# Optimization experiments

Measured on AMD Instinct MI355X. Metric: run time of the kernel, lower is better.

## Reference

```python
import jax, jax.numpy as jnp
import numpy as np

B, C, H, W = 1, 512, 64, 64
HEADS, DH = 8, 64
DI = HEADS * DH          # 512 = heads * dim_head
SW = 8                   # sliding window size
CB = 16                  # compress block size
SB = 2                   # selection block size
NSEL = 2                 # num selected blocks
N = H * W                # 4096 tokens
NCB = N // CB            # 256 compress blocks
NFB = N // SB            # 2048 fine (selection) blocks
NEG = jnp.finfo(jnp.float32).min


def setup_inputs() -> dict:
    key = jax.random.key(0)
    ks = jax.random.split(key, 24)
    rn = lambda k, shape, s=0.03: jax.random.normal(k, shape, jnp.float32) * s
    return dict(
        x=jax.random.normal(ks[0], (B, C, H, W), jnp.float32),
        w_in=rn(ks[1], (C, C)), b_in=jnp.zeros((C,), jnp.float32),
        g_norm=jnp.ones((C,), jnp.float32),
        wq=rn(ks[2], (DI, C)), wk=rn(ks[3], (DI, C)), wv=rn(ks[4], (DI, C)),
        k_pos=rn(ks[5], (HEADS, CB, DH), 0.02), v_pos=rn(ks[6], (HEADS, CB, DH), 0.02),
        mem_k=rn(ks[7], (HEADS, 1, DH), 0.02), mem_v=rn(ks[8], (HEADS, 1, DH), 0.02),
        kc_w1=rn(ks[9], (CB * DH, CB * DH)), kc_b1=jnp.zeros((CB * DH,), jnp.float32),
        kc_w2=rn(ks[10], (DH, CB * DH)), kc_b2=jnp.zeros((DH,), jnp.float32),
        vc_w1=rn(ks[11], (CB * DH, CB * DH)), vc_b1=jnp.zeros((CB * DH,), jnp.float32),
        vc_w2=rn(ks[12], (DH, CB * DH)), vc_b2=jnp.zeros((DH,), jnp.float32),
        w_strat=rn(ks[13], (3 * HEADS, C)), b_strat=jnp.zeros((3 * HEADS,), jnp.float32),
        w_comb=rn(ks[14], (C, DI)),
        w_out=rn(ks[15], (C, C)), b_out=jnp.zeros((C,), jnp.float32),
    )


def _rope(x):
    # rotary-embedding-torch default: theta=10000, interleaved pairs
    d = x.shape[-1]
    inv = 1.0 / (10000.0 ** (jnp.arange(0, d, 2, dtype=jnp.float32) / d))
    ang = jnp.arange(x.shape[-2], dtype=jnp.float32)[:, None] * inv  # (n, d/2)
    cos = jnp.repeat(jnp.cos(ang), 2, axis=-1)
    sin = jnp.repeat(jnp.sin(ang), 2, axis=-1)
    xp = x.reshape(x.shape[:-1] + (d // 2, 2))
    xr = jnp.stack((-xp[..., 1], xp[..., 0]), axis=-1).reshape(x.shape)
    return x * cos + xr * sin


def reference(x, w_in, b_in, g_norm, wq, wk, wv, k_pos, v_pos, mem_k, mem_v,
              kc_w1, kc_b1, kc_w2, kc_b2, vc_w1, vc_b1, vc_w2, vc_b2,
              w_strat, b_strat, w_comb, w_out, b_out):
    scale = DH ** -0.5
    # proj_in (1x1 conv) then flatten to sequence (b, n, c); residual uses this
    xs = jnp.einsum('bchw,oc->bohw', x, w_in) + b_in[None, :, None, None]
    seq = xs.reshape(B, C, N).transpose(0, 2, 1)
    # RMSNorm
    h = seq * jax.lax.rsqrt(jnp.mean(seq * seq, -1, keepdims=True) + 1e-6) * g_norm
    # qkv -> (b, heads, n, d)
    q = (h @ wq.T).reshape(B, N, HEADS, DH).transpose(0, 2, 1, 3)
    k = (h @ wk.T).reshape(B, N, HEADS, DH).transpose(0, 2, 1, 3)
    v = (h @ wv.T).reshape(B, N, HEADS, DH).transpose(0, 2, 1, 3)

    # ---- 1. compressed attention (block compression MLP + mem kv) ----
    kin = (k + jnp.tile(k_pos, (1, NCB, 1))[None]).reshape(B, HEADS, NCB, CB * DH)
    vin = (v + jnp.tile(v_pos, (1, NCB, 1))[None]).reshape(B, HEADS, NCB, CB * DH)
    ck = jax.nn.relu(kin @ kc_w1.T + kc_b1) @ kc_w2.T + kc_b2   # (b,h,NCB,d)
    cv = jax.nn.relu(vin @ vc_w1.T + vc_b1) @ vc_w2.T + vc_b2
    ck = jnp.concatenate([jnp.broadcast_to(mem_k[None], (B, HEADS, 1, DH)), ck], axis=2)
    cv = jnp.concatenate([jnp.broadcast_to(mem_v[None], (B, HEADS, 1, DH)), cv], axis=2)
    ck_seq = jnp.concatenate([jnp.array([-1]), (jnp.arange(NCB) + 1) * CB - 1])
    cmask = ck_seq[None, :] < jnp.arange(N)[:, None]             # (N, NCB+1), True=attend
    csim = jnp.einsum('bhid,bhjd->bhij', q, ck) * scale
    csim = jnp.where(cmask[None, None], csim, NEG)
    compressed_out = jnp.einsum('bhij,bhjd->bhid', jax.nn.softmax(csim, axis=-1), cv)

    # rotary positions for fine + sliding branches
    rq, rk = _rope(q), _rope(k)

    # ---- 2. fine selection attention ----
    # importance at fine-block granularity; since SB divides CB, each fine block
    # maps to exactly one compress block (equivalent to repeat->mask->mean in torch)
    imp = csim[..., 1:]                                          # drop mem kv logits
    fb_of = jnp.arange(NFB) // (CB // SB)
    imp_fine = imp[..., fb_of]                                   # (b,h,N,NFB)
    blk_causal = jnp.arange(NFB)[None, :] < (jnp.arange(N) // SB)[:, None]
    imp_fine = jnp.where(blk_causal[None, None], imp_fine, -jnp.inf)
    logits = jnp.concatenate([jnp.full((B, HEADS, N, 1), -1e3, jnp.float32), imp_fine], axis=-1)
    probs = jax.nn.softmax(logits, axis=-1)[..., 1:]             # (b,h,N,NFB)
    sel_val, sel_idx = jax.lax.top_k(probs, NSEL)                # (b,h,N,NSEL)
    diag_idx = jnp.broadcast_to((jnp.arange(N) // SB)[None, None, :, None], (B, HEADS, N, 1))
    sel_idx = jnp.concatenate([sel_idx, diag_idx], axis=-1)      # append own (diagonal) block
    fmask_sel = jnp.repeat((sel_val > 1e-10)[..., None], SB, axis=-1)   # (b,h,N,NSEL,SB)
    diag_mask = jnp.arange(SB)[None, :] <= (jnp.arange(N) % SB)[:, None]  # within-block causal
    diag_mask = jnp.broadcast_to(diag_mask[None, None, :, None, :], (B, HEADS, N, 1, SB))
    fmask = jnp.concatenate([fmask_sel, diag_mask], axis=-2).reshape(B, HEADS, N, (NSEL + 1) * SB)
    fk_blk = rk.reshape(B, HEADS, NFB, SB, DH)
    fv_blk = v.reshape(B, HEADS, NFB, SB, DH)
    idx = sel_idx.reshape(B, HEADS, N * (NSEL + 1))[..., None, None]
    fk = jnp.take_along_axis(fk_blk, idx, axis=2).reshape(B, HEADS, N, (NSEL + 1) * SB, DH)
    fv = jnp.take_along_axis(fv_blk, idx, axis=2).reshape(B, HEADS, N, (NSEL + 1) * SB, DH)
    fsim = jnp.einsum('bhid,bhijd->bhij', rq, fk) * scale
    fsim = jnp.where(fmask, fsim, NEG)
    fine_out = jnp.einsum('bhij,bhijd->bhid', jax.nn.softmax(fsim, axis=-1), fv)

    # ---- 3. sliding window attention (causal, exact window: 0 <= i-j <= SW) ----
    kp = jnp.pad(rk, ((0, 0), (0, 0), (SW, 0), (0, 0)))
    vp = jnp.pad(v, ((0, 0), (0, 0), (SW, 0), (0, 0)))
    widx = jnp.arange(N)[:, None] + jnp.arange(SW + 1)[None, :]  # indices into padded seq
    kw = kp[:, :, widx]                                          # (b,h,N,SW+1,d)
    vw = vp[:, :, widx]
    wvalid = (jnp.arange(N)[:, None] - SW + jnp.arange(SW + 1)[None, :]) >= 0
    ssim = jnp.einsum('bhid,bhijd->bhij', rq, kw) * scale
    ssim = jnp.where(wvalid[None, None], ssim, NEG)
    slide_out = jnp.einsum('bhij,bhijd->bhid', jax.nn.softmax(ssim, axis=-1), vw)

    # ---- combine the three strategies with learned sigmoid gates ----
    gates = jax.nn.sigmoid(h @ w_strat.T + b_strat).reshape(B, N, HEADS, 3).transpose(0, 2, 1, 3)
    out = gates[..., 0:1] * compressed_out + gates[..., 1:2] * fine_out + gates[..., 2:3] * slide_out
    out = out.transpose(0, 2, 1, 3).reshape(B, N, DI) @ w_comb.T  # merge heads + combine
    out2d = out.transpose(0, 2, 1).reshape(B, C, H, W)
    return jnp.einsum('bchw,oc->bohw', out2d, w_out) + b_out[None, :, None, None] + xs
```

## Files before the change

### kernel.cpp

```cpp
#include <hip/hip_runtime.h>
#include <hip/hip_bf16.h>
#include <math.h>

typedef __attribute__((ext_vector_type(8))) short s8v;
typedef __attribute__((ext_vector_type(8))) _Float16 h8v;
typedef __attribute__((ext_vector_type(4))) float f4v;
typedef __hip_bfloat16 bf16;

#define NEGF (-3.40282346638528859812e+38f)
#define QSMEM 20480
#define BSMEM 20480

enum { EPI_F32 = 0, EPI_BIAS, EPI_BRELU_BF16, EPI_BF16, EPI_FINAL };

__device__ __forceinline__ float wred_sum(float v) {
#pragma unroll
  for (int m = 1; m < 64; m <<= 1) v += __shfl_xor(v, m, 64);
  return v;
}

template <int EPI>
__device__ __forceinline__ void bgemm_body(char* smem, int bx, int by, int bz,
    const bf16* __restrict__ A, const bf16* __restrict__ B, void* __restrict__ C,
    int K, int ldC, long sA, long sB, long sC,
    const float* __restrict__ bias, const void* __restrict__ aux) {
  short (*Ahs)[2560] = (short(*)[2560])smem;
  short (*Bhs)[2560] = (short(*)[2560])(smem + 2 * 2560 * 2);
  const short* ah = (const short*)A + (long)bz * sA;
  const short* bh = (const short*)B + (long)bz * sB;
  int tid = threadIdx.x;
  int wv_ = tid >> 6, lane = tid & 63;
  int lrow = tid >> 2, lcol = (tid & 3) << 3;
  int lidx = lrow * 40 + lcol;
  long abase = (long)(bx * 64 + lrow) * K + lcol;
  long bbase = (long)(by * 64 + lrow) * K + lcol;
  int frow = lane & 15, fk = (lane >> 4) << 3;
  int aoff = (wv_ * 16 + frow) * 40 + fk;
  f4v acc[4] = {};
  {
    s8v avh = *(const s8v*)&ah[abase];
    s8v bvh = *(const s8v*)&bh[bbase];
    *(s8v*)&Ahs[0][lidx] = avh;
    *(s8v*)&Bhs[0][lidx] = bvh;
  }
  __syncthreads();
  int nit = K >> 5, buf = 0;
  s8v rAa, rAb, rBa, rBb;
  if (nit > 1) {
    rAa = *(const s8v*)&ah[abase + 32];
    rAb = *(const s8v*)&bh[bbase + 32];
  }
#define B_DSMFMA                                                       \
  {                                                                    \
    s8v afh = *(const s8v*)&Ahs[buf][aoff];                            \
    _Pragma("unroll") for (int nt = 0; nt < 4; nt++) {                 \
      s8v bfh = *(const s8v*)&Bhs[buf][(nt * 16 + frow) * 40 + fk];    \
      acc[nt] = __builtin_amdgcn_mfma_f32_16x16x32_bf16(afh, bfh, acc[nt], 0, 0, 0); \
    }                                                                  \
  }
  for (int it = 0; it < nit; it += 2) {
    if (it + 2 < nit) {
      long ko = (long)(it + 2) << 5;
      rBa = *(const s8v*)&ah[abase + ko];
      rBb = *(const s8v*)&bh[bbase + ko];
    }
    B_DSMFMA
    if (it + 1 < nit) {
      *(s8v*)&Ahs[buf ^ 1][lidx] = rAa;
      *(s8v*)&Bhs[buf ^ 1][lidx] = rAb;
      __syncthreads();
      buf ^= 1;
      if (it + 3 < nit) {
        long ko = (long)(it + 3) << 5;
        rAa = *(const s8v*)&ah[abase + ko];
        rAb = *(const s8v*)&bh[bbase + ko];
      }
      B_DSMFMA
      if (it + 2 < nit) {
        *(s8v*)&Ahs[buf ^ 1][lidx] = rBa;
        *(s8v*)&Bhs[buf ^ 1][lidx] = rBb;
        __syncthreads();
        buf ^= 1;
      }
    }
  }
#undef B_DSMFMA
  int rb = bx * 64 + wv_ * 16 + ((lane >> 4) << 2);
#pragma unroll
  for (int nt = 0; nt < 4; nt++) {
    int gn = by * 64 + nt * 16 + (lane & 15);
#pragma unroll
    for (int rg = 0; rg < 4; rg++) {
      int gm = rb + rg;
      float v = acc[nt][rg];
      long ci = (long)bz * sC + (long)gm * ldC + gn;
      if (EPI == EPI_F32) ((float*)C)[ci] = v;
      else if (EPI == EPI_BIAS) ((float*)C)[ci] = v + bias[gn];
      else if (EPI == EPI_BRELU_BF16) ((bf16*)C)[ci] = __float2bfloat16(fmaxf(v + bias[gn], 0.f));
      else if (EPI == EPI_BF16) ((bf16*)C)[ci] = __float2bfloat16(v);
      else if (EPI == EPI_FINAL)
        ((float*)C)[ci] = v + bias[gm] + ((const float*)aux)[(long)gn * 512 + gm];
    }
  }
}


#define HX_DECL                                                     \
  short* L = (short*)smem;                                          \
  const int MS = 64 * 40;                                           \
  int tid = threadIdx.x;                                            \
  int wv = tid >> 6, lane = tid & 63;                               \
  int lrow = tid >> 2, lcol = (tid & 3) << 3;                       \
  int frow = lane & 15, fk = (lane >> 4) << 3;                      \
  int aoff = (wv * 16 + frow) * 40 + fk;                            \
  int soff = lrow * 40 + lcol;                                      \
  f4v acc0[4] = {}, accx[4] = {}, acc2[4] = {};

#define HX_STAGE0                                                   \
  {                                                                 \
    *(h8v*)&L[0 * MS + soff] = *(const h8v*)&Ah[abase];             \
    *(h8v*)&L[1 * MS + soff] = *(const h8v*)&Al[abase];             \
    *(h8v*)&L[2 * MS + soff] = *(const h8v*)&Bh[bbase];             \
    *(h8v*)&L[3 * MS + soff] = *(const h8v*)&Bl[bbase];             \
  }                                                                 \
  __syncthreads();

#define HX_DSMFMA                                                   \
  {                                                                 \
    h8v ah = *(const h8v*)&L[aoff];                                 \
    h8v al = *(const h8v*)&L[MS + aoff];                            \
    _Pragma("unroll") for (int nt = 0; nt < 4; nt++) {              \
      int bo = 2 * MS + (nt * 16 + frow) * 40 + fk;                 \
      h8v bh = *(const h8v*)&L[bo];                                 \
      h8v bl = *(const h8v*)&L[bo + MS];                            \
      acc0[nt] = __builtin_amdgcn_mfma_f32_16x16x32_f16(ah, bh, acc0[nt], 0, 0, 0); \
      accx[nt] = __builtin_amdgcn_mfma_f32_16x16x32_f16(ah, bl, accx[nt], 0, 0, 0); \
      accx[nt] = __builtin_amdgcn_mfma_f32_16x16x32_f16(al, bh, accx[nt], 0, 0, 0); \
      acc2[nt] = __builtin_amdgcn_mfma_f32_16x16x32_f16(al, bl, acc2[nt], 0, 0, 0); \
    }                                                               \
  }

#define HX_LOOP(NIT)                                                \
  h8v rAa, rAb, rAc, rAd, rBa, rBb, rBc, rBd;                       \
  if ((NIT) > 1) {                                                  \
    rAa = *(const h8v*)&Ah[abase + 32];                             \
    rAb = *(const h8v*)&Al[abase + 32];                             \
    rAc = *(const h8v*)&Bh[bbase + 32];                             \
    rAd = *(const h8v*)&Bl[bbase + 32];                             \
  }                                                                 \
  for (int it = 0; it < (NIT); it += 2) {                           \
    if (it + 2 < (NIT)) {                                           \
      long ko = (long)(it + 2) << 5;                                \
      rBa = *(const h8v*)&Ah[abase + ko];                           \
      rBb = *(const h8v*)&Al[abase + ko];                           \
      rBc = *(const h8v*)&Bh[bbase + ko];                           \
      rBd = *(const h8v*)&Bl[bbase + ko];                           \
    }                                                               \
    HX_DSMFMA                                                       \
    if (it + 1 < (NIT)) {                                           \
      __syncthreads();                                              \
      *(h8v*)&L[soff] = rAa;                                        \
      *(h8v*)&L[MS + soff] = rAb;                                   \
      *(h8v*)&L[2 * MS + soff] = rAc;                               \
      *(h8v*)&L[3 * MS + soff] = rAd;                               \
      __syncthreads();                                              \
      if (it + 3 < (NIT)) {                                         \
        long ko = (long)(it + 3) << 5;                              \
        rAa = *(const h8v*)&Ah[abase + ko];                         \
        rAb = *(const h8v*)&Al[abase + ko];                         \
        rAc = *(const h8v*)&Bh[bbase + ko];                         \
        rAd = *(const h8v*)&Bl[bbase + ko];                         \
      }                                                             \
      HX_DSMFMA                                                     \
      if (it + 2 < (NIT)) {                                         \
        __syncthreads();                                            \
        *(h8v*)&L[soff] = rBa;                                      \
        *(h8v*)&L[MS + soff] = rBb;                                 \
        *(h8v*)&L[2 * MS + soff] = rBc;                             \
        *(h8v*)&L[3 * MS + soff] = rBd;                             \
        __syncthreads();                                            \
      }                                                             \
    }                                                               \
  }

#define HX_COMBINE(nt, rg) \
  (acc0[nt][rg] + (accx[nt][rg] + acc2[nt][rg] * (1.f / 4096.f)) * (1.f / 4096.f))

__device__ __forceinline__ void qk_f16_body(char* smem, int bx, int by,
    const _Float16* __restrict__ Ah, const _Float16* __restrict__ Al,
    const _Float16* __restrict__ Bh, const _Float16* __restrict__ Bl,
    _Float16* __restrict__ qhh, _Float16* __restrict__ qhl,
    _Float16* __restrict__ kinh, _Float16* __restrict__ kinl,
    float* __restrict__ rq, float* __restrict__ rk, const float* __restrict__ kpos,
    const float2* __restrict__ ropet) {
  HX_DECL
  long abase = (long)(bx * 64 + lrow) * 512 + lcol;
  long bbase = (long)(by * 64 + lrow) * 512 + lcol;
  HX_STAGE0
  HX_LOOP(16)
  bool isq = by < 8;
  int h = by & 7;
  int rb = wv * 16 + ((lane >> 4) << 2);
#pragma unroll
  for (int nt = 0; nt < 4; nt++) {
    int dloc = nt * 16 + frow;
    int d2 = dloc >> 1;
#pragma unroll
    for (int rg = 0; rg < 4; rg++) {
      int n = bx * 64 + rb + rg;
      float vf = HX_COMBINE(nt, rg);
      float2 cs = ropet[(long)n * 32 + d2];
      float sv = cs.x, cv = cs.y;
      float vp = __shfl_xor(vf, 1, 64);
      float rr = (dloc & 1) ? (vf * cv + vp * sv) : (vf * cv - vp * sv);
      long oi = ((long)h * 4096 + n) * 64 + dloc;
      if (isq) {
        _Float16 hi = (_Float16)vf;
        qhh[oi] = hi;
        qhl[oi] = (_Float16)((vf - (float)hi) * 4096.f);
        rq[oi] = rr;
      } else {
        rk[oi] = rr;
        float kv = vf + kpos[(h * 16 + (n & 15)) * 64 + dloc];
        _Float16 khi = (_Float16)kv;
        long ki = (((long)h * 256 + (n >> 4)) * 16 + (n & 15)) * 64 + dloc;
        kinh[ki] = khi;
        kinl[ki] = (_Float16)((kv - (float)khi) * 4096.f);
      }
    }
  }
}

__device__ __forceinline__ void hx_conv_body(char* smem, int bx, int by,
    const _Float16* __restrict__ Ah, const _Float16* __restrict__ Al,
    const _Float16* __restrict__ Bh, const _Float16* __restrict__ Bl,
    float* __restrict__ C, const float* __restrict__ bias) {
  HX_DECL
  long abase = (long)(bx * 64 + lrow) * 512 + lcol;
  long bbase = (long)(by * 64 + lrow) * 512 + lcol;
  HX_STAGE0
  HX_LOOP(16)
  int rb = bx * 64 + wv * 16 + ((lane >> 4) << 2);
#pragma unroll
  for (int nt = 0; nt < 4; nt++) {
    int gn = by * 64 + nt * 16 + frow;
#pragma unroll
    for (int rg = 0; rg < 4; rg++) {
      int gm = rb + rg;
      C[(long)gm * 512 + gn] = HX_COMBINE(nt, rg) + bias[gn];
    }
  }
}

__device__ __forceinline__ void hx_mlp1_body(char* smem, int bx, int by,
    const _Float16* __restrict__ Ah, const _Float16* __restrict__ Al,
    const _Float16* __restrict__ Bh, const _Float16* __restrict__ Bl,
    _Float16* __restrict__ Ch, _Float16* __restrict__ Cl, const float* __restrict__ bias) {
  HX_DECL
  long abase = (long)(bx * 64 + lrow) * 1024 + lcol;
  long bbase = (long)(by * 64 + lrow) * 1024 + lcol;
  HX_STAGE0
  HX_LOOP(32)
  int rb = bx * 64 + wv * 16 + ((lane >> 4) << 2);
#pragma unroll
  for (int nt = 0; nt < 4; nt++) {
    int gn = by * 64 + nt * 16 + frow;
#pragma unroll
    for (int rg = 0; rg < 4; rg++) {
      int gm = rb + rg;
      float v = fmaxf(HX_COMBINE(nt, rg) + bias[gn], 0.f);
      _Float16 hi = (_Float16)v;
      long ci = (long)gm * 1024 + gn;
      Ch[ci] = hi;
      Cl[ci] = (_Float16)((v - (float)hi) * 4096.f);
    }
  }
}

__device__ __forceinline__ void hx_ksplit_body(char* smem, int bx, int by,
    const _Float16* __restrict__ Ah, const _Float16* __restrict__ Al,
    const _Float16* __restrict__ Bh, const _Float16* __restrict__ Bl,
    float* __restrict__ P) {
  HX_DECL
  long kbeg = (long)by << 7;
  long abase = (long)(bx * 64 + lrow) * 1024 + kbeg + lcol;
  long bbase = (long)lrow * 1024 + kbeg + lcol;
  HX_STAGE0
  HX_LOOP(4)
  float* p = P + (long)by * 131072;
  int rb = bx * 64 + wv * 16 + ((lane >> 4) << 2);
#pragma unroll
  for (int nt = 0; nt < 4; nt++) {
    int gn = nt * 16 + frow;
#pragma unroll
    for (int rg = 0; rg < 4; rg++) {
      int gm = rb + rg;
      p[(long)gm * 64 + gn] = HX_COMBINE(nt, rg);
    }
  }
}

__device__ __forceinline__ void hx_csim_body(char* smem, int bx, int by, int bz,
    const _Float16* __restrict__ Ah, const _Float16* __restrict__ Al,
    const _Float16* __restrict__ Bh, const _Float16* __restrict__ Bl,
    float* __restrict__ C) {
  HX_DECL
  long abase = ((long)bz * 4096 + bx * 64 + lrow) * 64 + lcol;
  long bbase = ((long)bz * 320 + by * 64 + lrow) * 64 + lcol;
  HX_STAGE0
  HX_LOOP(2)
  int rb = bx * 64 + wv * 16 + ((lane >> 4) << 2);
#pragma unroll
  for (int nt = 0; nt < 4; nt++) {
    int gn = by * 64 + nt * 16 + frow;
#pragma unroll
    for (int rg = 0; rg < 4; rg++) {
      int gm = rb + rg;
      C[((long)bz * 4096 + gm) * 320 + gn] = HX_COMBINE(nt, rg) * 0.125f;
    }
  }
}

__device__ __forceinline__ void prep_elem(long i,
    const float* __restrict__ wq, const float* __restrict__ wk, const float* __restrict__ wv,
    const float* __restrict__ wst, const float* __restrict__ bst,
    const float* __restrict__ kc_w1, const float* __restrict__ kc_w2,
    const float* __restrict__ vc_w1, const float* __restrict__ vc_w2, const float* __restrict__ w_comb,
    const float* __restrict__ w_out, _Float16* __restrict__ wqkh, _Float16* __restrict__ wqkl,
    bf16* __restrict__ wvs, float* __restrict__ bias2,
    _Float16* __restrict__ kw1h, _Float16* __restrict__ kw1l,
    _Float16* __restrict__ kw2h, _Float16* __restrict__ kw2l, bf16* __restrict__ vw1b,
    bf16* __restrict__ vw2b, bf16* __restrict__ wcombb, bf16* __restrict__ woutb) {
  if (i < 524288) {
    int r = (int)(i >> 9), c = (int)(i & 511);
    float w = (r < 512) ? wq[i] : wk[(r - 512) * 512 + c];
    _Float16 hi = (_Float16)w;
    wqkh[i] = hi;
    wqkl[i] = (_Float16)((w - (float)hi) * 4096.f);
    return;
  }
  i -= 524288;
  if (i < 294912) {
    int r = (int)(i >> 9), c = (int)(i & 511);
    float v = 0.f;
    if (r < 512) v = wv[i];
    else if (r < 536) v = wst[(r - 512) * 512 + c];
    wvs[i] = __float2bfloat16(v);
    if (i < 576) bias2[i] = (i >= 512 && i < 536) ? bst[i - 512] : 0.f;
    return;
  }
  i -= 294912;
  if (i < 1048576) {
    float w = kc_w1[i];
    _Float16 hi = (_Float16)w;
    kw1h[i] = hi;
    kw1l[i] = (_Float16)((w - (float)hi) * 4096.f);
    return;
  }
  i -= 1048576;
  if (i < 65536) {
    float w = kc_w2[i];
    _Float16 hi = (_Float16)w;
    kw2h[i] = hi;
    kw2l[i] = (_Float16)((w - (float)hi) * 4096.f);
    return;
  }
  i -= 65536;
  if (i < 1048576) { vw1b[i] = __float2bfloat16(vc_w1[i]); return; }
  i -= 1048576;
  if (i < 65536) { vw2b[i] = __float2bfloat16(vc_w2[i]); return; }
  i -= 65536;
  if (i < 262144) { wcombb[i] = __float2bfloat16(w_comb[i]); return; }
  i -= 262144;
  if (i < 262144) woutb[i] = __float2bfloat16(w_out[i]);
}
#define PREP_TOTAL 3571712l

template <int EPI>
__global__ __launch_bounds__(256) void gemm_bt(
    const bf16* __restrict__ A, const bf16* __restrict__ B, void* __restrict__ C,
    int K, int ldC, long sA, long sB, long sC,
    const float* __restrict__ bias, const void* __restrict__ aux) {
  __shared__ char smem[BSMEM];
  bgemm_body<EPI>(smem, blockIdx.x, blockIdx.y, blockIdx.z, A, B, C, K, ldC, sA, sB, sC, bias, aux);
}

__global__ __launch_bounds__(256) void k_conv_prep(
    const _Float16* __restrict__ xth, const _Float16* __restrict__ xtl,
    const _Float16* __restrict__ winh, const _Float16* __restrict__ winl,
    float* __restrict__ xsf, const float* __restrict__ b_in,
    const float* __restrict__ wq, const float* __restrict__ wk, const float* __restrict__ wv,
    const float* __restrict__ wst, const float* __restrict__ bst,
    const float* __restrict__ kc_w1, const float* __restrict__ kc_w2,
    const float* __restrict__ vc_w1, const float* __restrict__ vc_w2, const float* __restrict__ w_comb,
    const float* __restrict__ w_out, _Float16* __restrict__ wqkh, _Float16* __restrict__ wqkl,
    bf16* __restrict__ wvs, float* __restrict__ bias2,
    _Float16* __restrict__ kw1h, _Float16* __restrict__ kw1l,
    _Float16* __restrict__ kw2h, _Float16* __restrict__ kw2l, bf16* __restrict__ vw1b,
    bf16* __restrict__ vw2b, bf16* __restrict__ wcombb, bf16* __restrict__ woutb) {
  __shared__ char smem[QSMEM];
  if (blockIdx.y < 8) {
    hx_conv_body(smem, blockIdx.x, blockIdx.y, xth, xtl, winh, winl, xsf, b_in);
  } else {
    long base = (((long)(blockIdx.y - 8) * 64 + blockIdx.x) * 256) + threadIdx.x;
    for (long i = base; i < PREP_TOTAL; i += 16l * 64 * 256)
      prep_elem(i, wq, wk, wv, wst, bst, kc_w1, kc_w2, vc_w1, vc_w2, w_comb, w_out,
                wqkh, wqkl, wvs, bias2, kw1h, kw1l, kw2h, kw2l, vw1b, vw2b, wcombb, woutb);
  }
}

__global__ __launch_bounds__(256) void k_fused_qk_t2(
    const _Float16* __restrict__ hhi, const _Float16* __restrict__ hlo,
    const _Float16* __restrict__ wqkh, const _Float16* __restrict__ wqkl,
    _Float16* __restrict__ qhh, _Float16* __restrict__ qhl,
    _Float16* __restrict__ kinh, _Float16* __restrict__ kinl,
    float* __restrict__ rq, float* __restrict__ rk, const float* __restrict__ kpos,
    const float2* __restrict__ ropet,
    const bf16* __restrict__ hbf, const bf16* __restrict__ wvs, float* __restrict__ T2,
    const float* __restrict__ bias2) {
  __shared__ char smem[QSMEM];
  if (blockIdx.y >= 16) {
    bgemm_body<EPI_BIAS>(smem, blockIdx.x, blockIdx.y - 16, 0, hbf, wvs, T2, 512, 576, 0, 0, 0, bias2,
                         nullptr);
    return;
  }
  qk_f16_body(smem, blockIdx.x, blockIdx.y, hhi, hlo, wqkh, wqkl, qhh, qhl, kinh, kinl, rq, rk, kpos,
              ropet);
}

__global__ void k_repackV(const float* __restrict__ T2, const float* __restrict__ vpos,
                          float* __restrict__ vvv, bf16* __restrict__ vin) {
  int e = blockIdx.x * 256 + threadIdx.x;
  int d = e & 63, n = (e >> 6) & 4095, h = e >> 18;
  float v0 = T2[(long)n * 576 + h * 64 + d];
  vvv[((long)h * 4096 + n) * 64 + d] = v0;
  vin[(((long)h * 256 + (n >> 4)) * 16 + (n & 15)) * 64 + d] =
      __float2bfloat16(v0 + vpos[(h * 16 + (n & 15)) * 64 + d]);
}

__global__ __launch_bounds__(256) void k_fused_mlp1(
    const _Float16* __restrict__ kinh, const _Float16* __restrict__ kinl,
    const _Float16* __restrict__ kw1h, const _Float16* __restrict__ kw1l,
    _Float16* __restrict__ hidh, _Float16* __restrict__ hidl, const float* __restrict__ kb1,
    const bf16* __restrict__ vin, const bf16* __restrict__ vw1,
    bf16* __restrict__ hidv, const float* __restrict__ vb1) {
  __shared__ char smem[QSMEM];
  if (blockIdx.y < 16)
    hx_mlp1_body(smem, blockIdx.x, blockIdx.y, kinh, kinl, kw1h, kw1l, hidh, hidl, kb1);
  else
    bgemm_body<EPI_BRELU_BF16>(smem, blockIdx.x, blockIdx.y - 16, 0, vin, vw1, hidv, 1024, 1024, 0, 0, 0,
                               vb1, nullptr);
}

__global__ __launch_bounds__(256) void k_fused_mlp2(
    const _Float16* __restrict__ hidh, const _Float16* __restrict__ hidl,
    const _Float16* __restrict__ kw2h, const _Float16* __restrict__ kw2l, float* __restrict__ kpart,
    const bf16* __restrict__ hidv, const bf16* __restrict__ vw2, float* __restrict__ cvc,
    const float* __restrict__ vb2) {
  __shared__ char smem[QSMEM];
  if (blockIdx.y < 8)
    hx_ksplit_body(smem, blockIdx.x, blockIdx.y, hidh, hidl, kw2h, kw2l, kpart);
  else
    bgemm_body<EPI_BIAS>(smem, blockIdx.x, 0, 0, hidv, vw2, cvc, 1024, 64, 0, 0, 0, vb2, nullptr);
}

__global__ __launch_bounds__(256) void k_csim(
    const _Float16* __restrict__ qhh, const _Float16* __restrict__ qhl,
    const _Float16* __restrict__ ckbh, const _Float16* __restrict__ ckbl, float* __restrict__ csim) {
  if (blockIdx.y * 64 > blockIdx.x * 4 + 3) return;
  __shared__ char smem[QSMEM];
  hx_csim_body(smem, blockIdx.x, blockIdx.y, blockIdx.z, qhh, qhl, ckbh, ckbl, csim);
}

__global__ void k_transpose16(const float* __restrict__ x, _Float16* __restrict__ xth,
                              _Float16* __restrict__ xtl,
                              const float* __restrict__ w_in, _Float16* __restrict__ winh,
                              _Float16* __restrict__ winl, float2* __restrict__ ropet) {
  if (blockIdx.y == 16) {
    int tid = threadIdx.y * 32 + threadIdx.x;
    long base = (long)blockIdx.x * 256 + tid;
    for (long i = base; i < 393216; i += 128l * 256) {
      if (i < 262144) {
        float w = w_in[i];
        _Float16 hi = (_Float16)w;
        winh[i] = hi;
        winl[i] = (_Float16)((w - (float)hi) * 4096.f);
      } else {
        int idx = (int)(i - 262144);
        int d2 = idx & 31, n = idx >> 5;
        float inv = exp2f((float)d2 * -0.4152410118609203f);
        float sv, cv;
        sincosf((float)n * inv, &sv, &cv);
        ropet[idx] = make_float2(sv, cv);
      }
    }
    return;
  }
  __shared__ float t[32][33];
  int n0 = blockIdx.x * 32, c0 = blockIdx.y * 32;
  int tx = threadIdx.x, ty = threadIdx.y;
#pragma unroll
  for (int r = ty; r < 32; r += 8) t[r][tx] = x[(long)(c0 + r) * 4096 + n0 + tx];
  __syncthreads();
#pragma unroll
  for (int r = ty; r < 32; r += 8) {
    float v = t[tx][r];
    _Float16 hi = (_Float16)v;
    long o = (long)(n0 + r) * 512 + c0 + tx;
    xth[o] = hi;
    xtl[o] = (_Float16)((v - (float)hi) * 4096.f);
  }
}

__global__ __launch_bounds__(256) void k_rmsnorm(const float* __restrict__ xs, const float* __restrict__ g,
                                                 _Float16* __restrict__ hhi, _Float16* __restrict__ hlo,
                                                 bf16* __restrict__ hbf) {
  int n = blockIdx.x, t = threadIdx.x;
  const float* row = xs + (long)n * 512;
  double a = (double)row[t], b = (double)row[t + 256];
  double ss = a * a + b * b;
#pragma unroll
  for (int m = 1; m < 64; m <<= 1) ss += __shfl_xor(ss, m, 64);
  __shared__ double red[4];
  if ((t & 63) == 0) red[t >> 6] = ss;
  __syncthreads();
  double tot = red[0] + red[1] + red[2] + red[3];
  double r = 1.0 / sqrt(tot / 512.0 + 1e-6);
  double h0 = a * r * (double)g[t], h1 = b * r * (double)g[t + 256];
  long o = (long)n * 512 + t;
  float f0 = (float)h0, f1 = (float)h1;
  _Float16 a0 = (_Float16)f0, a1 = (_Float16)f1;
  hhi[o] = a0;
  hhi[o + 256] = a1;
  hlo[o] = (_Float16)((f0 - (float)a0) * 4096.f);
  hlo[o + 256] = (_Float16)((f1 - (float)a1) * 4096.f);
  hbf[o] = __float2bfloat16(f0);
  hbf[o + 256] = __float2bfloat16(f1);
}

__global__ void k_repackB(const float* __restrict__ kpart, const float* __restrict__ cvc,
                          const float* __restrict__ mem_k, const float* __restrict__ mem_v,
                          const float* __restrict__ kb2, _Float16* __restrict__ ckbh,
                          _Float16* __restrict__ ckbl, bf16* __restrict__ cvtb) {
  int g = blockIdx.x * 256 + threadIdx.x;
  if (g < 8 * 320 * 64) {
    int d = g & 63, j = (g >> 6) % 320, h = g / (320 * 64);
    float vf = 0.f;
    if (j == 0) vf = mem_k[h * 64 + d];
    else if (j < 257) {
      long ri = ((long)h * 256 + (j - 1)) * 64 + d;
      double s = 0.0;
#pragma unroll
      for (int p = 0; p < 8; p++) s += (double)kpart[(long)p * 131072 + ri];
      vf = (float)(s + (double)kb2[d]);
    }
    _Float16 hi = (_Float16)vf;
    ckbh[g] = hi;
    ckbl[g] = (_Float16)((vf - (float)hi) * 4096.f);
  }
  if (g < 8 * 64 * 288) {
    int j = g % 288, d = (g / 288) & 63, h = g / (288 * 64);
    float v = 0.f;
    if (j == 0) v = mem_v[h * 64 + d];
    else if (j < 257) v = cvc[((long)h * 256 + (j - 1)) * 64 + d];
    cvtb[g] = __float2bfloat16(v);
  }
}

__global__ __launch_bounds__(256) void k_selsm(const float* __restrict__ csim, bf16* __restrict__ pb,
                                               int4* __restrict__ selb) {
  int r = blockIdx.x * 4 + (threadIdx.x >> 6);
  int lane = threadIdx.x & 63;
  int i = r & 4095;
  const float* row = csim + (long)r * 320;
  int nv = i / 16 + 1;
  float s[5], e[5];
  float mx = -INFINITY;
#pragma unroll
  for (int t = 0; t < 5; t++) {
    int j = lane + 64 * t;
    float v = (j < nv) ? row[j] : -INFINITY;
    s[t] = v;
    mx = fmaxf(mx, v);
  }
#pragma unroll
  for (int m = 1; m < 64; m <<= 1) mx = fmaxf(mx, __shfl_xor(mx, m, 64));
  float sum = 0.f;
#pragma unroll
  for (int t = 0; t < 5; t++) {
    int j = lane + 64 * t;
    e[t] = (j < nv) ? __expf(s[t] - mx) : 0.f;
    sum += e[t];
  }
  sum = wred_sum(sum);
  float rinv = 1.f / sum;
  bf16* prow = pb + (long)r * 288;
#pragma unroll
  for (int t = 0; t < 5; t++) {
    int j = lane + 64 * t;
    if (j < 288) prow[j] = __float2bfloat16((j < nv) ? e[t] * rinv : 0.f);
  }
  int nvb = i >> 1;
  int nmv = (nvb + 7) >> 3;
  float vm[4];
  float bestv = -INFINITY;
  int bestm = 0x7fffffff;
#pragma unroll
  for (int t = 0; t < 4; t++) {
    int m = lane + 64 * t;
    float v = -INFINITY;
    if (m < nmv) v = (m + 1 < nv) ? row[m + 1] : NEGF;
    vm[t] = v;
    if (v > bestv) { bestv = v; bestm = m; }
  }
#pragma unroll
  for (int mk = 1; mk < 64; mk <<= 1) {
    float ov = __shfl_xor(bestv, mk, 64);
    int om = __shfl_xor(bestm, mk, 64);
    if (ov > bestv || (ov == bestv && om < bestm)) { bestv = ov; bestm = om; }
  }
  int m0 = bestm;
  int cnt0 = min(8, nvb - 8 * m0);
  float rv = -INFINITY;
  int rm = 0x7fffffff;
#pragma unroll
  for (int t = 0; t < 4; t++) {
    int m = lane + 64 * t;
    if (m != m0 && vm[t] > rv) { rv = vm[t]; rm = m; }
  }
#pragma unroll
  for (int mk = 1; mk < 64; mk <<= 1) {
    float ov = __shfl_xor(rv, mk, 64);
    int om = __shfl_xor(rm, mk, 64);
    if (ov > rv || (ov == rv && om < rm)) { rv = ov; rm = om; }
  }
  float Ml = fmaxf(-1000.f, bestv);
  float z = 0.f;
#pragma unroll
  for (int t = 0; t < 4; t++) {
    int m = lane + 64 * t;
    if (m < nmv) z += (float)min(8, nvb - 8 * m) * expf(vm[t] - Ml);
  }
  z = wred_sum(z) + expf(-1000.f - Ml);
  int fb0 = 0, fb1 = 0, mk0 = 0, mk1 = 0;
  if (nmv > 0) {
    float sv0 = expf(bestv - Ml) / z;
    fb0 = 8 * m0;
    mk0 = sv0 > 1e-10f;
    if (cnt0 >= 2) { fb1 = fb0 + 1; mk1 = mk0; }
    else if (nmv > 1) {
      float sv1 = expf(rv - Ml) / z;
      fb1 = 8 * rm;
      mk1 = sv1 > 1e-10f;
    }
  }
  if (lane == 0) selb[r] = make_int4(fb0, fb1, mk0, mk1);
}

__global__ __launch_bounds__(256) void k_fineslide(const float* __restrict__ rq, const float* __restrict__ rk,
                                                   const float* __restrict__ vv, const float* __restrict__ co,
                                                   const int4* __restrict__ selb, const float* __restrict__ T2,
                                                   bf16* __restrict__ comb) {
  int r = blockIdx.x * 4 + (threadIdx.x >> 6);
  int d = threadIdx.x & 63;
  int h = r >> 12, i = r & 4095;
  long hb = (long)h * 4096 * 64;
  float qd = rq[hb + (long)i * 64 + d];
  int4 s4 = selb[r];
  int dg = i >> 1;
  int tok[6] = {2 * s4.x, 2 * s4.x + 1, 2 * s4.y, 2 * s4.y + 1, 2 * dg, 2 * dg + 1};
  int ok6[6] = {s4.z, s4.z, s4.w, s4.w, 1, (i & 1)};
  float sim[6], val[6];
#pragma unroll
  for (int j = 0; j < 6; j++) {
    float kd = rk[hb + (long)tok[j] * 64 + d];
    val[j] = vv[hb + (long)tok[j] * 64 + d];
    float p = wred_sum(qd * kd);
    sim[j] = ok6[j] ? p * 0.125f : NEGF;
  }
  float mx = sim[0];
#pragma unroll
  for (int j = 1; j < 6; j++) mx = fmaxf(mx, sim[j]);
  float den = 0.f, fo = 0.f;
#pragma unroll
  for (int j = 0; j < 6; j++) {
    float e_ = __expf(sim[j] - mx);
    den += e_;
    fo += e_ * val[j];
  }
  fo /= den;
  float ssim[9], sval[9];
#pragma unroll
  for (int t = 0; t < 9; t++) {
    int tk = i - 8 + t;
    int okt = tk >= 0;
    int tc = okt ? tk : 0;
    float kd = rk[hb + (long)tc * 64 + d];
    sval[t] = okt ? vv[hb + (long)tc * 64 + d] : 0.f;
    float p = wred_sum(qd * kd);
    ssim[t] = okt ? p * 0.125f : NEGF;
  }
  float mx2 = ssim[8];
#pragma unroll
  for (int t = 0; t < 8; t++) mx2 = fmaxf(mx2, ssim[t]);
  float den2 = 0.f, so = 0.f;
#pragma unroll
  for (int t = 0; t < 9; t++) {
    float e_ = __expf(ssim[t] - mx2);
    den2 += e_;
    so += e_ * sval[t];
  }
  so /= den2;
  const float* gb = T2 + (long)i * 576 + 512 + h * 3;
  float g0 = 1.f / (1.f + __expf(-gb[0]));
  float g1 = 1.f / (1.f + __expf(-gb[1]));
  float g2 = 1.f / (1.f + __expf(-gb[2]));
  float cd = co[hb + (long)i * 64 + d];
  comb[(long)i * 512 + h * 64 + d] = __float2bfloat16(g0 * cd + g1 * fo + g2 * so);
}

extern "C" void kernel_launch(void* const* d_in, const int* in_sizes, int n_in, void* d_out, int out_size,
                              void* d_ws, size_t ws_size, hipStream_t stream) {
  (void)in_sizes; (void)n_in; (void)out_size; (void)ws_size;
  const float* x = (const float*)d_in[0];
  const float* w_in = (const float*)d_in[1];
  const float* b_in = (const float*)d_in[2];
  const float* g_norm = (const float*)d_in[3];
  const float* wq = (const float*)d_in[4];
  const float* wk = (const float*)d_in[5];
  const float* wv = (const float*)d_in[6];
  const float* k_pos = (const float*)d_in[7];
  const float* v_pos = (const float*)d_in[8];
  const float* mem_k = (const float*)d_in[9];
  const float* mem_v = (const float*)d_in[10];
  const float* kc_w1 = (const float*)d_in[11];
  const float* kc_b1 = (const float*)d_in[12];
  const float* kc_w2 = (const float*)d_in[13];
  const float* kc_b2 = (const float*)d_in[14];
  const float* vc_w1 = (const float*)d_in[15];
  const float* vc_b1 = (const float*)d_in[16];
  const float* vc_w2 = (const float*)d_in[17];
  const float* vc_b2 = (const float*)d_in[18];
  const float* w_strat = (const float*)d_in[19];
  const float* b_strat = (const float*)d_in[20];
  const float* w_comb = (const float*)d_in[21];
  const float* w_out = (const float*)d_in[22];
  const float* b_out = (const float*)d_in[23];

  char* wsp = (char*)d_ws;
  size_t off = 0;
  auto alloc = [&](size_t b) -> void* {
    void* p = wsp + off;
    off += (b + 255) & ~(size_t)255;
    return p;
  };
  float* xsf = (float*)alloc(4096l * 512 * 4);
  _Float16* hhi = (_Float16*)alloc(4096l * 512 * 2);
  _Float16* hlo = (_Float16*)alloc(4096l * 512 * 2);
  bf16* hbf = (bf16*)alloc(4096l * 512 * 2);
  _Float16* winh = (_Float16*)alloc(512l * 512 * 2);
  _Float16* winl = (_Float16*)alloc(512l * 512 * 2);
  _Float16* wqkh = (_Float16*)alloc(1024l * 512 * 2);
  _Float16* wqkl = (_Float16*)alloc(1024l * 512 * 2);
  bf16* wvs = (bf16*)alloc(576l * 512 * 2);
  float* bias2 = (float*)alloc(576 * 4);
  float2* ropet = (float2*)alloc(4096l * 32 * 8);
  float* T2 = (float*)alloc(4096l * 576 * 4);
  float* csim = (float*)alloc(8l * 4096 * 320 * 4);
  _Float16* qhh = (_Float16*)alloc(8l * 4096 * 64 * 2);
  _Float16* qhl = (_Float16*)alloc(8l * 4096 * 64 * 2);
  float* rq = (float*)alloc(8l * 4096 * 64 * 4);
  float* rk = (float*)alloc(8l * 4096 * 64 * 4);
  float* vvb = (float*)alloc(8l * 4096 * 64 * 4);
  char* xthl = (char*)alloc(2l * 4096 * 512 * 2);
  _Float16* xth = (_Float16*)xthl;
  _Float16* xtl = xth + 4096l * 512;
  _Float16* hidh = xth;
  _Float16* hidl = xtl;
  char* kinpb = (char*)alloc(2048l * 1024 * 8 + 2048l * 1024 * 2);
  _Float16* kinh = (_Float16*)kinpb;
  _Float16* kinl = kinh + 2048l * 1024;
  bf16* vinb = (bf16*)(kinpb + 2l * 2048 * 1024 * 2);
  bf16* pb = (bf16*)kinpb;
  _Float16* kw1h = (_Float16*)alloc(1024l * 1024 * 2);
  _Float16* kw1l = (_Float16*)alloc(1024l * 1024 * 2);
  _Float16* kw2h = (_Float16*)alloc(64l * 1024 * 2);
  _Float16* kw2l = (_Float16*)alloc(64l * 1024 * 2);
  bf16* vw1b = (bf16*)alloc(1024l * 1024 * 2);
  bf16* vw2b = (bf16*)alloc(64l * 1024 * 2);
  bf16* hidv = (bf16*)alloc(2048l * 1024 * 2);
  float* cvc = (float*)alloc(2048l * 64 * 4);
  _Float16* ckbh = (_Float16*)alloc(8l * 320 * 64 * 2);
  _Float16* ckbl = (_Float16*)alloc(8l * 320 * 64 * 2);
  bf16* cvtb = (bf16*)alloc(8l * 64 * 288 * 2);
  int4* selb = (int4*)alloc(32768l * 16);
  float* co = (float*)alloc(8l * 4096 * 64 * 4);
  bf16* comb = (bf16*)alloc(4096l * 512 * 2);
  bf16* zb = (bf16*)alloc(4096l * 512 * 2);
  bf16* wcombb = (bf16*)alloc(512l * 512 * 2);
  bf16* woutb = (bf16*)alloc(512l * 512 * 2);
  float* kpart = (float*)alloc(8l * 2048 * 64 * 4);

  k_transpose16<<<dim3(128, 17), dim3(32, 8), 0, stream>>>(x, xth, xtl, w_in, winh, winl, ropet);
  k_conv_prep<<<dim3(64, 24), 256, 0, stream>>>(xth, xtl, winh, winl, xsf, b_in, wq, wk, wv, w_strat,
                                                b_strat, kc_w1, kc_w2, vc_w1, vc_w2, w_comb, w_out,
                                                wqkh, wqkl, wvs, bias2, kw1h, kw1l, kw2h, kw2l,
                                                vw1b, vw2b, wcombb, woutb);
  k_rmsnorm<<<4096, 256, 0, stream>>>(xsf, g_norm, hhi, hlo, hbf);
  k_fused_qk_t2<<<dim3(64, 25, 1), 256, 0, stream>>>(hhi, hlo, wqkh, wqkl, qhh, qhl, kinh, kinl, rq, rk,
                                                     k_pos, ropet, hbf, wvs, T2, bias2);
  k_repackV<<<8192, 256, 0, stream>>>(T2, v_pos, vvb, vinb);
  k_fused_mlp1<<<dim3(32, 32, 1), 256, 0, stream>>>(kinh, kinl, kw1h, kw1l, hidh, hidl, kc_b1, vinb, vw1b,
                                                    hidv, vc_b1);
  k_fused_mlp2<<<dim3(32, 9, 1), 256, 0, stream>>>(hidh, hidl, kw2h, kw2l, kpart, hidv, vw2b, cvc, vc_b2);
  k_repackB<<<640, 256, 0, stream>>>(kpart, cvc, mem_k, mem_v, kc_b2, ckbh, ckbl, cvtb);
  k_csim<<<dim3(64, 5, 8), 256, 0, stream>>>(qhh, qhl, ckbh, ckbl, csim);
  k_selsm<<<8192, 256, 0, stream>>>(csim, pb, selb);
  gemm_bt<EPI_F32><<<dim3(64, 1, 8), 256, 0, stream>>>(pb, cvtb, co, 288, 64, 4096l * 288, 64l * 288,
                                                       4096l * 64, nullptr, nullptr);
  k_fineslide<<<8192, 256, 0, stream>>>(rq, rk, vvb, co, selb, T2, comb);
  gemm_bt<EPI_BF16><<<dim3(64, 8, 1), 256, 0, stream>>>(comb, wcombb, zb, 512, 512, 0, 0, 0, nullptr, nullptr);
  gemm_bt<EPI_FINAL><<<dim3(8, 64, 1), 256, 0, stream>>>(woutb, zb, d_out, 512, 4096, 0, 0, 0, b_out, xsf);
}
```

Baseline: 325.6 us.

## Load GEMM A operand directly to registers and drop lo*lo split-precision term

The A tile in the bf16 and split-f16 GEMMs is now read from global memory straight into MFMA fragment registers. It is no longer staged through shared memory, which halves LDS size and LDS traffic. The split-f16 GEMMs also drop the al*bl MFMA product, whose contribution is scaled by 2^-24, removing a quarter of the MFMAs. The costs are slightly lower accuracy and less coalesced global loads for A.

```diff
diff --git a/kernel.cpp b/kernel.cpp
--- a/kernel.cpp
+++ b/kernel.cpp
@@ -8,8 +8,8 @@
 typedef __hip_bfloat16 bf16;
 
 #define NEGF (-3.40282346638528859812e+38f)
-#define QSMEM 20480
-#define BSMEM 20480
+#define QSMEM 10240
+#define BSMEM 10240
 
 enum { EPI_F32 = 0, EPI_BIAS, EPI_BRELU_BF16, EPI_BF16, EPI_FINAL };
 
@@ -24,67 +24,52 @@
     const bf16* __restrict__ A, const bf16* __restrict__ B, void* __restrict__ C,
     int K, int ldC, long sA, long sB, long sC,
     const float* __restrict__ bias, const void* __restrict__ aux) {
-  short (*Ahs)[2560] = (short(*)[2560])smem;
-  short (*Bhs)[2560] = (short(*)[2560])(smem + 2 * 2560 * 2);
+  short (*Bhs)[2560] = (short(*)[2560])smem;
   const short* ah = (const short*)A + (long)bz * sA;
   const short* bh = (const short*)B + (long)bz * sB;
   int tid = threadIdx.x;
   int wv_ = tid >> 6, lane = tid & 63;
   int lrow = tid >> 2, lcol = (tid & 3) << 3;
   int lidx = lrow * 40 + lcol;
-  long abase = (long)(bx * 64 + lrow) * K + lcol;
   long bbase = (long)(by * 64 + lrow) * K + lcol;
   int frow = lane & 15, fk = (lane >> 4) << 3;
-  int aoff = (wv_ * 16 + frow) * 40 + fk;
+  long aga = (long)(bx * 64 + wv_ * 16 + frow) * K + fk;
   f4v acc[4] = {};
-  {
-    s8v avh = *(const s8v*)&ah[abase];
-    s8v bvh = *(const s8v*)&bh[bbase];
-    *(s8v*)&Ahs[0][lidx] = avh;
-    *(s8v*)&Bhs[0][lidx] = bvh;
-  }
+  { *(s8v*)&Bhs[0][lidx] = *(const s8v*)&bh[bbase]; }
   __syncthreads();
   int nit = K >> 5, buf = 0;
-  s8v rAa, rAb, rBa, rBb;
+  s8v rA, rB, sE, sO;
+  sE = *(const s8v*)&ah[aga];
   if (nit > 1) {
-    rAa = *(const s8v*)&ah[abase + 32];
-    rAb = *(const s8v*)&bh[bbase + 32];
-  }
-#define B_DSMFMA                                                       \
+    rA = *(const s8v*)&bh[bbase + 32];
+    sO = *(const s8v*)&ah[aga + 32];
+  }
+#define B_MFMA(sreg)                                                   \
   {                                                                    \
-    s8v afh = *(const s8v*)&Ahs[buf][aoff];                            \
     _Pragma("unroll") for (int nt = 0; nt < 4; nt++) {                 \
       s8v bfh = *(const s8v*)&Bhs[buf][(nt * 16 + frow) * 40 + fk];    \
-      acc[nt] = __builtin_amdgcn_mfma_f32_16x16x32_bf16(afh, bfh, acc[nt], 0, 0, 0); \
+      acc[nt] = __builtin_amdgcn_mfma_f32_16x16x32_bf16(sreg, bfh, acc[nt], 0, 0, 0); \
     }                                                                  \
   }
   for (int it = 0; it < nit; it += 2) {
-    if (it + 2 < nit) {
-      long ko = (long)(it + 2) << 5;
-      rBa = *(const s8v*)&ah[abase + ko];
-      rBb = *(const s8v*)&bh[bbase + ko];
-    }
-    B_DSMFMA
+    if (it + 2 < nit) rB = *(const s8v*)&bh[bbase + ((long)(it + 2) << 5)];
+    B_MFMA(sE)
+    if (it + 2 < nit) sE = *(const s8v*)&ah[aga + ((long)(it + 2) << 5)];
     if (it + 1 < nit) {
-      *(s8v*)&Ahs[buf ^ 1][lidx] = rAa;
-      *(s8v*)&Bhs[buf ^ 1][lidx] = rAb;
+      *(s8v*)&Bhs[buf ^ 1][lidx] = rA;
       __syncthreads();
       buf ^= 1;
-      if (it + 3 < nit) {
-        long ko = (long)(it + 3) << 5;
-        rAa = *(const s8v*)&ah[abase + ko];
-        rAb = *(const s8v*)&bh[bbase + ko];
-      }
-      B_DSMFMA
+      if (it + 3 < nit) rA = *(const s8v*)&bh[bbase + ((long)(it + 3) << 5)];
+      B_MFMA(sO)
+      if (it + 3 < nit) sO = *(const s8v*)&ah[aga + ((long)(it + 3) << 5)];
       if (it + 2 < nit) {
-        *(s8v*)&Ahs[buf ^ 1][lidx] = rBa;
-        *(s8v*)&Bhs[buf ^ 1][lidx] = rBb;
+        *(s8v*)&Bhs[buf ^ 1][lidx] = rB;
         __syncthreads();
         buf ^= 1;
       }
     }
   }
-#undef B_DSMFMA
+#undef B_MFMA
   int rb = bx * 64 + wv_ * 16 + ((lane >> 4) << 2);
 #pragma unroll
   for (int nt = 0; nt < 4; nt++) {
@@ -112,79 +97,76 @@
   int wv = tid >> 6, lane = tid & 63;                               \
   int lrow = tid >> 2, lcol = (tid & 3) << 3;                       \
   int frow = lane & 15, fk = (lane >> 4) << 3;                      \
-  int aoff = (wv * 16 + frow) * 40 + fk;                            \
   int soff = lrow * 40 + lcol;                                      \
-  f4v acc0[4] = {}, accx[4] = {}, acc2[4] = {};
+  f4v acc0[4] = {}, accx[4] = {};
 
 #define HX_STAGE0                                                   \
   {                                                                 \
-    *(h8v*)&L[0 * MS + soff] = *(const h8v*)&Ah[abase];             \
-    *(h8v*)&L[1 * MS + soff] = *(const h8v*)&Al[abase];             \
-    *(h8v*)&L[2 * MS + soff] = *(const h8v*)&Bh[bbase];             \
-    *(h8v*)&L[3 * MS + soff] = *(const h8v*)&Bl[bbase];             \
+    *(h8v*)&L[soff] = *(const h8v*)&Bh[bbase];                      \
+    *(h8v*)&L[MS + soff] = *(const h8v*)&Bl[bbase];                 \
   }                                                                 \
   __syncthreads();
 
-#define HX_DSMFMA                                                   \
+#define HX_MFMA(sah, sal)                                           \
   {                                                                 \
-    h8v ah = *(const h8v*)&L[aoff];                                 \
-    h8v al = *(const h8v*)&L[MS + aoff];                            \
     _Pragma("unroll") for (int nt = 0; nt < 4; nt++) {              \
-      int bo = 2 * MS + (nt * 16 + frow) * 40 + fk;                 \
-      h8v bh = *(const h8v*)&L[bo];                                 \
-      h8v bl = *(const h8v*)&L[bo + MS];                            \
-      acc0[nt] = __builtin_amdgcn_mfma_f32_16x16x32_f16(ah, bh, acc0[nt], 0, 0, 0); \
-      accx[nt] = __builtin_amdgcn_mfma_f32_16x16x32_f16(ah, bl, accx[nt], 0, 0, 0); \
-      accx[nt] = __builtin_amdgcn_mfma_f32_16x16x32_f16(al, bh, accx[nt], 0, 0, 0); \
-      acc2[nt] = __builtin_amdgcn_mfma_f32_16x16x32_f16(al, bl, acc2[nt], 0, 0, 0); \
+      int bo = (nt * 16 + frow) * 40 + fk;                          \
+      h8v bh_ = *(const h8v*)&L[bo];                                \
+      h8v bl_ = *(const h8v*)&L[MS + bo];                           \
+      acc0[nt] = __builtin_amdgcn_mfma_f32_16x16x32_f16(sah, bh_, acc0[nt], 0, 0, 0); \
+      accx[nt] = __builtin_amdgcn_mfma_f32_16x16x32_f16(sah, bl_, accx[nt], 0, 0, 0); \
+      accx[nt] = __builtin_amdgcn_mfma_f32_16x16x32_f16(sal, bh_, accx[nt], 0, 0, 0); \
     }                                                               \
   }
 
 #define HX_LOOP(NIT)                                                \
-  h8v rAa, rAb, rAc, rAd, rBa, rBb, rBc, rBd;                       \
+  h8v rAh, rAl, rBh, rBl, sEh, sEl, sOh, sOl;                       \
+  sEh = *(const h8v*)&Ah[aga];                                      \
+  sEl = *(const h8v*)&Al[aga];                                      \
   if ((NIT) > 1) {                                                  \
-    rAa = *(const h8v*)&Ah[abase + 32];                             \
-    rAb = *(const h8v*)&Al[abase + 32];                             \
-    rAc = *(const h8v*)&Bh[bbase + 32];                             \
-    rAd = *(const h8v*)&Bl[bbase + 32];                             \
+    rAh = *(const h8v*)&Bh[bbase + 32];                             \
+    rAl = *(const h8v*)&Bl[bbase + 32];                             \
+    sOh = *(const h8v*)&Ah[aga + 32];                               \
+    sOl = *(const h8v*)&Al[aga + 32];                               \
   }                                                                 \
   for (int it = 0; it < (NIT); it += 2) {                           \
     if (it + 2 < (NIT)) {                                           \
       long ko = (long)(it + 2) << 5;                                \
-      rBa = *(const h8v*)&Ah[abase + ko];                           \
-      rBb = *(const h8v*)&Al[abase + ko];                           \
-      rBc = *(const h8v*)&Bh[bbase + ko];                           \
-      rBd = *(const h8v*)&Bl[bbase + ko];                           \
+      rBh = *(const h8v*)&Bh[bbase + ko];                           \
+      rBl = *(const h8v*)&Bl[bbase + ko];                           \
     }                                                               \
-    HX_DSMFMA                                                       \
+    HX_MFMA(sEh, sEl)                                               \
+    if (it + 2 < (NIT)) {                                           \
+      long ko = (long)(it + 2) << 5;                                \
+      sEh = *(const h8v*)&Ah[aga + ko];                             \
+      sEl = *(const h8v*)&Al[aga + ko];                             \
+    }                                                               \
     if (it + 1 < (NIT)) {                                           \
       __syncthreads();                                              \
-      *(h8v*)&L[soff] = rAa;                                        \
-      *(h8v*)&L[MS + soff] = rAb;                                   \
-      *(h8v*)&L[2 * MS + soff] = rAc;                               \
-      *(h8v*)&L[3 * MS + soff] = rAd;                               \
+      *(h8v*)&L[soff] = rAh;                                        \
+      *(h8v*)&L[MS + soff] = rAl;                                   \
       __syncthreads();                                              \
       if (it + 3 < (NIT)) {                                         \
         long ko = (long)(it + 3) << 5;                              \
-        rAa = *(const h8v*)&Ah[abase + ko];                         \
-        rAb = *(const h8v*)&Al[abase + ko];                         \
-        rAc = *(const h8v*)&Bh[bbase + ko];                         \
-        rAd = *(const h8v*)&Bl[bbase + ko];                         \
+        rAh = *(const h8v*)&Bh[bbase + ko];                         \
+        rAl = *(const h8v*)&Bl[bbase + ko];                         \
       }                                                             \
-      HX_DSMFMA                                                     \
+      HX_MFMA(sOh, sOl)                                             \
+      if (it + 3 < (NIT)) {                                         \
+        long ko = (long)(it + 3) << 5;                              \
+        sOh = *(const h8v*)&Ah[aga + ko];                           \
+        sOl = *(const h8v*)&Al[aga + ko];                           \
+      }                                                             \
       if (it + 2 < (NIT)) {                                         \
         __syncthreads();                                            \
-        *(h8v*)&L[soff] = rBa;                                      \
-        *(h8v*)&L[MS + soff] = rBb;                                 \
-        *(h8v*)&L[2 * MS + soff] = rBc;                             \
-        *(h8v*)&L[3 * MS + soff] = rBd;                             \
+        *(h8v*)&L[soff] = rBh;                                      \
+        *(h8v*)&L[MS + soff] = rBl;                                 \
         __syncthreads();                                            \
       }                                                             \
     }                                                               \
   }
 
-#define HX_COMBINE(nt, rg) \
-  (acc0[nt][rg] + (accx[nt][rg] + acc2[nt][rg] * (1.f / 4096.f)) * (1.f / 4096.f))
+#define HX_COMBINE(nt, rg) (acc0[nt][rg] + accx[nt][rg] * (1.f / 4096.f))
 
 __device__ __forceinline__ void qk_f16_body(char* smem, int bx, int by,
     const _Float16* __restrict__ Ah, const _Float16* __restrict__ Al,
@@ -194,7 +176,7 @@
     float* __restrict__ rq, float* __restrict__ rk, const float* __restrict__ kpos,
     const float2* __restrict__ ropet) {
   HX_DECL
-  long abase = (long)(bx * 64 + lrow) * 512 + lcol;
+  long aga = (long)(bx * 64 + wv * 16 + frow) * 512 + fk;
   long bbase = (long)(by * 64 + lrow) * 512 + lcol;
   HX_STAGE0
   HX_LOOP(16)
@@ -236,7 +218,7 @@
     const _Float16* __restrict__ Bh, const _Float16* __restrict__ Bl,
     float* __restrict__ C, const float* __restrict__ bias) {
   HX_DECL
-  long abase = (long)(bx * 64 + lrow) * 512 + lcol;
+  long aga = (long)(bx * 64 + wv * 16 + frow) * 512 + fk;
   long bbase = (long)(by * 64 + lrow) * 512 + lcol;
   HX_STAGE0
   HX_LOOP(16)
@@ -257,7 +239,7 @@
     const _Float16* __restrict__ Bh, const _Float16* __restrict__ Bl,
     _Float16* __restrict__ Ch, _Float16* __restrict__ Cl, const float* __restrict__ bias) {
   HX_DECL
-  long abase = (long)(bx * 64 + lrow) * 1024 + lcol;
+  long aga = (long)(bx * 64 + wv * 16 + frow) * 1024 + fk;
   long bbase = (long)(by * 64 + lrow) * 1024 + lcol;
   HX_STAGE0
   HX_LOOP(32)
@@ -283,7 +265,7 @@
     float* __restrict__ P) {
   HX_DECL
   long kbeg = (long)by << 7;
-  long abase = (long)(bx * 64 + lrow) * 1024 + kbeg + lcol;
+  long aga = (long)(bx * 64 + wv * 16 + frow) * 1024 + kbeg + fk;
   long bbase = (long)lrow * 1024 + kbeg + lcol;
   HX_STAGE0
   HX_LOOP(4)
@@ -305,7 +287,7 @@
     const _Float16* __restrict__ Bh, const _Float16* __restrict__ Bl,
     float* __restrict__ C) {
   HX_DECL
-  long abase = ((long)bz * 4096 + bx * 64 + lrow) * 64 + lcol;
+  long aga = ((long)bz * 4096 + bx * 64 + wv * 16 + frow) * 64 + fk;
   long bbase = ((long)bz * 320 + by * 64 + lrow) * 64 + lcol;
   HX_STAGE0
   HX_LOOP(2)
```

Result: slower. 332.7 us (+2.2%).
